# Kernel optimization log

Hardware: AMD Instinct MI355X
Metric: run time of the kernel (lower is better)

The kernel has to match this reference:

```python
import jax, jax.numpy as jnp
import numpy as np

B, L, E, H, V, NC = 64, 256, 300, 128, 50000, 2
NH1, F1 = 8, 8  # GAT layer 1: 8 heads x 8 features; layer 2: 1 head x 1 feature
LRELU = 0.2


def _lstm_dir(x, W, U, b):
    # x: [B, L, E]; W: [4H, E]; U: [4H, H]; b: [4H] (b_ih + b_hh fused)
    Bq, Hq = x.shape[0], U.shape[1]
    def step(carry, xt):
        h, c = carry
        g = xt @ W.T + h @ U.T + b
        i, f, gg, o = jnp.split(g, 4, axis=-1)  # PyTorch gate order i,f,g,o
        c = jax.nn.sigmoid(f) * c + jax.nn.sigmoid(i) * jnp.tanh(gg)
        h = jax.nn.sigmoid(o) * jnp.tanh(c)
        return (h, c), h
    h0 = jnp.zeros((Bq, Hq), x.dtype)
    _, hs = jax.lax.scan(step, (h0, h0), jnp.swapaxes(x, 0, 1))
    return jnp.swapaxes(hs, 0, 1)  # [B, L, H]


def bilstm(x, Wf, Uf, bf, Wb, Ub, bb):
    hf = _lstm_dir(x, Wf, Uf, bf)
    hb = _lstm_dir(x[:, ::-1], Wb, Ub, bb)[:, ::-1]
    return jnp.concatenate([hf, hb], axis=-1)  # [B, L, 2H]


def gat_layer(x, W, a_src, a_trg, bias, n_heads, f_out, concat, elu_act):
    # Dense equivalent of GAT IMP3 on a fully-connected graph (edge (s,t): src=s, trg=t).
    Bq, Lq, _ = x.shape
    proj = (x @ W.T).reshape(Bq, Lq, n_heads, f_out)        # [B,L,NH,F]
    s_src = jnp.einsum('blhf,hf->blh', proj, a_src)          # [B,L,NH]
    s_trg = jnp.einsum('blhf,hf->blh', proj, a_trg)
    sc = jax.nn.leaky_relu(s_src[:, :, None, :] + s_trg[:, None, :, :], LRELU)  # [B,S,T,NH]
    m = jnp.max(sc, axis=(1, 2, 3), keepdims=True)           # global max per graph (as in IMP3)
    e = jnp.exp(sc - m)
    A = e / (jnp.sum(e, axis=1, keepdims=True) + 1e-16)      # softmax over sources per target
    out = jnp.einsum('bsth,bshf->bthf', A, proj)             # scatter-aggregate to targets
    if concat:
        out = out.reshape(Bq, Lq, n_heads * f_out)
    else:
        out = out.mean(axis=2)
    out = out + bias
    if elu_act:
        out = jax.nn.elu(out)
    return out, A


def setup_inputs() -> dict:
    key = jax.random.key(0)
    ks = jax.random.split(key, 20)
    n = lambda k, shape, s=0.05: (jax.random.normal(k, shape, jnp.float32) * s)
    return {
        'input_ids': jax.random.randint(ks[0], (B, L), 0, V, jnp.int32),
        'attention_mask': jnp.ones((B, L), bool),
        'emb': n(ks[1], (V, E), 0.1),
        'Wih_f': n(ks[2], (4 * H, E)), 'Whh_f': n(ks[3], (4 * H, H)), 'b_f': jnp.zeros((4 * H,), jnp.float32),
        'Wih_b': n(ks[4], (4 * H, E)), 'Whh_b': n(ks[5], (4 * H, H)), 'b_b': jnp.zeros((4 * H,), jnp.float32),
        'g1_W': n(ks[6], (NH1 * F1, 2 * H)), 'g1_src': n(ks[7], (NH1, F1), 0.1), 'g1_trg': n(ks[8], (NH1, F1), 0.1), 'g1_b': jnp.zeros((NH1 * F1,), jnp.float32),
        'g2_W': n(ks[9], (1, NH1 * F1)), 'g2_src': n(ks[10], (1, 1), 0.1), 'g2_trg': n(ks[11], (1, 1), 0.1), 'g2_b': jnp.zeros((1,), jnp.float32),
        'ctx': n(ks[12], (L, 1), 0.1),
        'lin_W': n(ks[13], (B, 2 * H)), 'lin_b': jnp.zeros((B,), jnp.float32),
        'out_W': n(ks[14], (NC, B)), 'out_b': jnp.zeros((NC,), jnp.float32),
    }


def reference(input_ids, attention_mask, emb, Wih_f, Whh_f, b_f, Wih_b, Whh_b, b_b,
              g1_W, g1_src, g1_trg, g1_b, g2_W, g2_src, g2_trg, g2_b,
              ctx, lin_W, lin_b, out_W, out_b):
    x = emb[input_ids]                                   # [B,L,E] (dropout = eval no-op)
    h_seq = bilstm(x, Wih_f, Whh_f, b_f, Wih_b, Whh_b, b_b)  # [B,L,2H]
    h1, _ = gat_layer(h_seq, g1_W, g1_src, g1_trg, g1_b, NH1, F1, True, True)
    _, A2 = gat_layer(h1, g2_W, g2_src, g2_trg, g2_b, 1, 1, False, False)
    att2 = A2[..., 0]                                    # [B, src, trg] == att.view(-1, 2H) rows
    att = jnp.einsum('bst,t->bs', att2, ctx[:, 0])       # mm with context_vector
    att = jnp.where(attention_mask, att, -jnp.inf)
    att = jax.nn.softmax(att, axis=1)                    # [B,L]
    pooled = jnp.max(h_seq * att[..., None], axis=1)     # [B,2H]
    hcl = jax.nn.relu(pooled @ lin_W.T + lin_b)
    logits = hcl @ out_W.T + out_b                       # [B,NC]
    return (logits, att)
```

## Files before the change

### kernel.cpp

```cpp
#include <hip/hip_runtime.h>
#include <math.h>
#include <stdint.h>

#define Bq 64
#define Lq 256
#define Eq 300
#define Hq 128
#define MQ (Bq*Lq)

#define LRELU_S 0.2f

__device__ __forceinline__ float lrelu(float x) { return x > 0.f ? x : LRELU_S * x; }

typedef short short8 __attribute__((ext_vector_type(8)));
typedef float f32x4v __attribute__((ext_vector_type(4)));

__device__ __forceinline__ unsigned short f2bf(float x) {
  unsigned u = __float_as_uint(x);
  u += 0x7FFFu + ((u >> 16) & 1u);
  return (unsigned short)(u >> 16);
}
__device__ __forceinline__ float bf2f(unsigned short h) {
  return __uint_as_float(((unsigned)h) << 16);
}

#define BM 64
#define BN 64
#define BK 16

__global__ __launch_bounds__(256) void gemm_awt(
    const float* __restrict__ Asrc, const int* __restrict__ ids,
    const float* __restrict__ W, const float* __restrict__ bias,
    float* __restrict__ C, int M, int N, int K)
{
  __shared__ float As[BK][BM + 4];
  __shared__ float Bs[BK][BN + 4];
  int tid = threadIdx.x;
  int tx = tid & 15, ty = tid >> 4;
  int row0 = blockIdx.x * BM, col0 = blockIdx.y * BN;

  int lrow = tid >> 2;
  int lk   = (tid & 3) << 2;

  const float* Arow;
  {
    int r = row0 + lrow;
    int id = ids ? ids[r] : r;
    Arow = Asrc + (size_t)id * K;
  }
  const float* Wrow = W + (size_t)(col0 + lrow) * K;

  float acc[4][4] = {};

  for (int k0 = 0; k0 < K; k0 += BK) {
    int kk = k0 + lk;
    float4 av, bv;
    if (kk + 3 < K) {
      av = *(const float4*)(Arow + kk);
      bv = *(const float4*)(Wrow + kk);
    } else {
      float a0 = (kk + 0 < K) ? Arow[kk + 0] : 0.f;
      float a1 = (kk + 1 < K) ? Arow[kk + 1] : 0.f;
      float a2 = (kk + 2 < K) ? Arow[kk + 2] : 0.f;
      float a3 = (kk + 3 < K) ? Arow[kk + 3] : 0.f;
      av = make_float4(a0, a1, a2, a3);
      float b0 = (kk + 0 < K) ? Wrow[kk + 0] : 0.f;
      float b1 = (kk + 1 < K) ? Wrow[kk + 1] : 0.f;
      float b2 = (kk + 2 < K) ? Wrow[kk + 2] : 0.f;
      float b3 = (kk + 3 < K) ? Wrow[kk + 3] : 0.f;
      bv = make_float4(b0, b1, b2, b3);
    }
    As[lk + 0][lrow] = av.x; As[lk + 1][lrow] = av.y;
    As[lk + 2][lrow] = av.z; As[lk + 3][lrow] = av.w;
    Bs[lk + 0][lrow] = bv.x; Bs[lk + 1][lrow] = bv.y;
    Bs[lk + 2][lrow] = bv.z; Bs[lk + 3][lrow] = bv.w;
    __syncthreads();

    #pragma unroll
    for (int k = 0; k < BK; ++k) {
      float4 a4 = *(const float4*)&As[k][ty * 4];
      float4 b4 = *(const float4*)&Bs[k][tx * 4];
      float a[4] = {a4.x, a4.y, a4.z, a4.w};
      float bb[4] = {b4.x, b4.y, b4.z, b4.w};
      #pragma unroll
      for (int i = 0; i < 4; ++i)
        #pragma unroll
        for (int j = 0; j < 4; ++j)
          acc[i][j] += a[i] * bb[j];
    }
    __syncthreads();
  }

  #pragma unroll
  for (int i = 0; i < 4; ++i) {
    int r = row0 + ty * 4 + i;
    #pragma unroll
    for (int j = 0; j < 4; ++j) {
      int cidx = col0 + tx * 4 + j;
      float v = acc[i][j] + (bias ? bias[cidx] : 0.f);
      C[(size_t)r * N + cidx] = v;
    }
  }
}

__global__ __launch_bounds__(256) void gemm_gates_mfma(
    const float* __restrict__ emb, const int* __restrict__ ids,
    const float* __restrict__ Wf, const float* __restrict__ bf,
    const float* __restrict__ Wb, const float* __restrict__ bb_,
    float* __restrict__ C)
{
  __shared__ __align__(16) short Ah[128 * 32];
  __shared__ __align__(16) short Al[128 * 32];
  __shared__ __align__(16) short Bh[128 * 32];
  __shared__ __align__(16) short Bl[128 * 32];
  __shared__ int ids_s[128];

  int tid = threadIdx.x;
  int row0 = blockIdx.x * 128;
  int col0 = blockIdx.y * 128;
  const float* W    = (col0 < 512) ? Wf : Wb;
  const float* bias = (col0 < 512) ? bf : bb_;
  int wcol0 = col0 & 511;

  if (tid < 128) ids_s[tid] = ids[row0 + tid];
  __syncthreads();

  int l  = tid & 63, wv = tid >> 6;
  int wm = wv >> 1,  wn = wv & 1;
  int kq = l >> 4,   rl = l & 15;

  f32x4v acc[4][4] = {};

  for (int k0 = 0; k0 < 300; k0 += 32) {
    #pragma unroll
    for (int p = 0; p < 4; ++p) {
      int idx = p * 256 + tid;
      int row = idx >> 3, c4 = idx & 7;
      int gk = k0 + c4 * 4;
      float4 av = make_float4(0.f, 0.f, 0.f, 0.f);
      float4 bv = make_float4(0.f, 0.f, 0.f, 0.f);
      if (gk < 300) {
        av = *(const float4*)(emb + (size_t)ids_s[row] * 300 + gk);
        bv = *(const float4*)(W + (size_t)(wcol0 + row) * 300 + gk);
      }
      int chunk = (c4 >> 1) ^ ((row >> 2) & 3);
      int off = row * 32 + chunk * 8 + (c4 & 1) * 4;
      {
        unsigned short h0 = f2bf(av.x), h1 = f2bf(av.y), h2 = f2bf(av.z), h3 = f2bf(av.w);
        unsigned short l0 = f2bf(av.x - bf2f(h0)), l1 = f2bf(av.y - bf2f(h1));
        unsigned short l2 = f2bf(av.z - bf2f(h2)), l3 = f2bf(av.w - bf2f(h3));
        uint2 ph; ph.x = (unsigned)h0 | ((unsigned)h1 << 16); ph.y = (unsigned)h2 | ((unsigned)h3 << 16);
        uint2 pl; pl.x = (unsigned)l0 | ((unsigned)l1 << 16); pl.y = (unsigned)l2 | ((unsigned)l3 << 16);
        *(uint2*)&Ah[off] = ph;
        *(uint2*)&Al[off] = pl;
      }
      {
        unsigned short h0 = f2bf(bv.x), h1 = f2bf(bv.y), h2 = f2bf(bv.z), h3 = f2bf(bv.w);
        unsigned short l0 = f2bf(bv.x - bf2f(h0)), l1 = f2bf(bv.y - bf2f(h1));
        unsigned short l2 = f2bf(bv.z - bf2f(h2)), l3 = f2bf(bv.w - bf2f(h3));
        uint2 ph; ph.x = (unsigned)h0 | ((unsigned)h1 << 16); ph.y = (unsigned)h2 | ((unsigned)h3 << 16);
        uint2 pl; pl.x = (unsigned)l0 | ((unsigned)l1 << 16); pl.y = (unsigned)l2 | ((unsigned)l3 << 16);
        *(uint2*)&Bh[off] = ph;
        *(uint2*)&Bl[off] = pl;
      }
    }
    __syncthreads();

    short8 ah[4], al_[4], bh[4], bl[4];
    #pragma unroll
    for (int f = 0; f < 4; ++f) {
      int ar = wm * 64 + f * 16 + rl;
      int ac = kq ^ ((ar >> 2) & 3);
      ah[f]  = *(const short8*)&Ah[ar * 32 + ac * 8];
      al_[f] = *(const short8*)&Al[ar * 32 + ac * 8];
      int br = wn * 64 + f * 16 + rl;
      int bc = kq ^ ((br >> 2) & 3);
      bh[f]  = *(const short8*)&Bh[br * 32 + bc * 8];
      bl[f]  = *(const short8*)&Bl[br * 32 + bc * 8];
    }
    #pragma unroll
    for (int fm = 0; fm < 4; ++fm)
      #pragma unroll
      for (int fn = 0; fn < 4; ++fn) {
        acc[fm][fn] = __builtin_amdgcn_mfma_f32_16x16x32_bf16(ah[fm],  bh[fn], acc[fm][fn], 0, 0, 0);
        acc[fm][fn] = __builtin_amdgcn_mfma_f32_16x16x32_bf16(ah[fm],  bl[fn], acc[fm][fn], 0, 0, 0);
        acc[fm][fn] = __builtin_amdgcn_mfma_f32_16x16x32_bf16(al_[fm], bh[fn], acc[fm][fn], 0, 0, 0);
      }
    __syncthreads();
  }

  int fq = l >> 4;
  #pragma unroll
  for (int fm = 0; fm < 4; ++fm) {
    #pragma unroll
    for (int fn = 0; fn < 4; ++fn) {
      int gr = row0 + wm * 64 + fm * 16 + fq * 4;
      int lc = wn * 64 + fn * 16 + rl;
      float bsv = bias[wcol0 + lc];
      #pragma unroll
      for (int i = 0; i < 4; ++i)
        C[(size_t)(gr + i) * 1024 + col0 + lc] = acc[fm][fn][i] + bsv;
    }
  }
}

#define MVB(s0,s1,s2,s3, u0,u1,u2,u3, off) \
  "s_waitcnt lgkmcnt(5)\n" \
  "v_fmac_f32 v88, v" #s0 ", v" #u0 "\n" \
  "v_fmac_f32 v89, v" #s1 ", v" #u1 "\n" \
  "v_fmac_f32 v90, v" #s2 ", v" #u2 "\n" \
  "v_fmac_f32 v91, v" #s3 ", v" #u3 "\n" \
  "ds_read_b128 v[" #s0 ":" #s3 "], v81 offset:" #off "\n"

#define MVT(n, s0,s1,s2,s3, u0,u1,u2,u3) \
  "s_waitcnt lgkmcnt(" #n ")\n" \
  "v_fmac_f32 v88, v" #s0 ", v" #u0 "\n" \
  "v_fmac_f32 v89, v" #s1 ", v" #u1 "\n" \
  "v_fmac_f32 v90, v" #s2 ", v" #u2 "\n" \
  "v_fmac_f32 v91, v" #s3 ", v" #u3 "\n"

#define ULD(lo,hi,off) \
  "global_load_dwordx4 v[" #lo ":" #hi "], v80, %[ub] offset:" #off "\n"

__global__ __launch_bounds__(512, 1) void lstm_kernel(
    const float* __restrict__ ws_base,
    const float* __restrict__ Uf, const float* __restrict__ Ub,
    float* __restrict__ h_seq)
{
  __shared__ __align__(1024) float h_sh[2][Hq];
  int blk = blockIdx.x;
  int b = blk & 63;
  int dir = blk >> 6;
  int j = threadIdx.x;
  int lane = j & 63;
  int w = j >> 6;
  int gate = (lane >> 4) & 3;
  int hidx = (w << 4) | (lane & 15);
  int row = (gate << 7) | hidx;

  const float* U = dir ? Ub : Uf;
  int tt0 = dir ? (Lq - 1) : 0;

  unsigned uo  = (unsigned)row * (Hq * 4u);
  unsigned go0 = (1024u + (unsigned)(b * Lq + tt0) * 1024u
                  + (unsigned)dir * 512u + (unsigned)row) * 4u;
  unsigned ho0 = ((unsigned)(b * Lq + tt0) * 256u
                  + (unsigned)dir * (unsigned)Hq + (unsigned)hidx) * 4u;
  int gd = dir ? -4096 : 4096;
  int hd = dir ? -1024 : 1024;

  unsigned lds_base = (unsigned)(uintptr_t)&h_sh[0][0];
  unsigned ldsr0 = lds_base;
  unsigned ldsw0 = lds_base + 512u + (unsigned)hidx * 4u;

  bool isg = (gate == 2);
  float klog = isg ? -2.8853900817779268f : -1.4426950408889634f;
  float mc = isg ? 2.f : 1.f;
  float ac = isg ? -1.f : 0.f;
  int base4 = (lane & 15) * 4;
  int bp0 = base4, bp1 = base4 + 64, bp2 = base4 + 128, bp3 = base4 + 192;

  if (j < Hq) h_sh[0][j] = 0.f;
  __syncthreads();

  asm volatile(
    "v_mov_b32 v80, %[uo]\n"
    "v_mov_b32 v81, %[ldsr0]\n"
    "v_mov_b32 v82, %[ldsw0]\n"
    "v_mov_b32 v83, %[go0]\n"
    "v_mov_b32 v84, %[ho0]\n"
    "v_mov_b32 v87, 0\n"
    "s_mov_b32 s90, 0\n"
    ULD(128,131,0)   ULD(132,135,16)  ULD(136,139,32)  ULD(140,143,48)
    ULD(144,147,64)  ULD(148,151,80)  ULD(152,155,96)  ULD(156,159,112)
    ULD(160,163,128) ULD(164,167,144) ULD(168,171,160) ULD(172,175,176)
    ULD(176,179,192) ULD(180,183,208) ULD(184,187,224) ULD(188,191,240)
    ULD(192,195,256) ULD(196,199,272) ULD(200,203,288) ULD(204,207,304)
    ULD(208,211,320) ULD(212,215,336) ULD(216,219,352) ULD(220,223,368)
    ULD(224,227,384) ULD(228,231,400) ULD(232,235,416) ULD(236,239,432)
    ULD(240,243,448) ULD(244,247,464) ULD(248,251,480) ULD(252,255,496)
    "global_load_dword v85, v83, %[wsb]\n"
    "s_waitcnt vmcnt(0)\n"
    "Ltop_%=:\n"
    "v_add_u32 v83, %[gd], v83\n"
    "global_load_dword v86, v83, %[wsb]\n"
    "ds_read_b128 v[100:103], v81\n"
    "ds_read_b128 v[104:107], v81 offset:16\n"
    "ds_read_b128 v[108:111], v81 offset:32\n"
    "ds_read_b128 v[112:115], v81 offset:48\n"
    "ds_read_b128 v[116:119], v81 offset:64\n"
    "ds_read_b128 v[120:123], v81 offset:80\n"
    "v_mov_b32 v88, v85\n"
    "v_mov_b32 v89, 0\n"
    "v_mov_b32 v90, 0\n"
    "v_mov_b32 v91, 0\n"
    MVB(100,101,102,103, 128,129,130,131, 96)
    MVB(104,105,106,107, 132,133,134,135, 112)
    MVB(108,109,110,111, 136,137,138,139, 128)
    MVB(112,113,114,115, 140,141,142,143, 144)
    MVB(116,117,118,119, 144,145,146,147, 160)
    MVB(120,121,122,123, 148,149,150,151, 176)
    MVB(100,101,102,103, 152,153,154,155, 192)
    MVB(104,105,106,107, 156,157,158,159, 208)
    MVB(108,109,110,111, 160,161,162,163, 224)
    MVB(112,113,114,115, 164,165,166,167, 240)
    MVB(116,117,118,119, 168,169,170,171, 256)
    MVB(120,121,122,123, 172,173,174,175, 272)
    MVB(100,101,102,103, 176,177,178,179, 288)
    MVB(104,105,106,107, 180,181,182,183, 304)
    MVB(108,109,110,111, 184,185,186,187, 320)
    MVB(112,113,114,115, 188,189,190,191, 336)
    MVB(116,117,118,119, 192,193,194,195, 352)
    MVB(120,121,122,123, 196,197,198,199, 368)
    MVB(100,101,102,103, 200,201,202,203, 384)
    MVB(104,105,106,107, 204,205,206,207, 400)
    MVB(108,109,110,111, 208,209,210,211, 416)
    MVB(112,113,114,115, 212,213,214,215, 432)
    MVB(116,117,118,119, 216,217,218,219, 448)
    MVB(120,121,122,123, 220,221,222,223, 464)
    MVB(100,101,102,103, 224,225,226,227, 480)
    MVB(104,105,106,107, 228,229,230,231, 496)
    MVT(5, 108,109,110,111, 232,233,234,235)
    MVT(4, 112,113,114,115, 236,237,238,239)
    MVT(3, 116,117,118,119, 240,241,242,243)
    MVT(2, 120,121,122,123, 244,245,246,247)
    MVT(1, 100,101,102,103, 248,249,250,251)
    MVT(0, 104,105,106,107, 252,253,254,255)
    "v_add_f32 v88, v88, v90\n"
    "v_add_f32 v89, v89, v91\n"
    "v_add_f32 v88, v88, v89\n"
    "v_mul_f32 v92, %[klog], v88\n"
    "v_exp_f32 v93, v92\n"
    "s_nop 1\n"
    "v_add_f32 v94, 1.0, v93\n"
    "v_rcp_f32 v95, v94\n"
    "s_nop 1\n"
    "v_mul_f32 v96, v94, v95\n"
    "v_sub_f32 v96, 2.0, v96\n"
    "v_mul_f32 v95, v95, v96\n"
    "v_fma_f32 v97, v95, %[mc], %[ac]\n"
    "ds_bpermute_b32 v92, %[bp0], v97\n"
    "ds_bpermute_b32 v93, %[bp1], v97\n"
    "ds_bpermute_b32 v94, %[bp2], v97\n"
    "ds_bpermute_b32 v98, %[bp3], v97\n"
    "s_waitcnt lgkmcnt(0)\n"
    "v_mul_f32 v95, v92, v94\n"
    "v_fma_f32 v87, v93, v87, v95\n"
    "v_mul_f32 v92, 0xc038aa3b, v87\n"
    "v_exp_f32 v93, v92\n"
    "s_nop 1\n"
    "v_add_f32 v94, 1.0, v93\n"
    "v_rcp_f32 v95, v94\n"
    "s_nop 1\n"
    "v_mul_f32 v96, v94, v95\n"
    "v_sub_f32 v96, 2.0, v96\n"
    "v_mul_f32 v95, v95, v96\n"
    "v_fma_f32 v96, v95, 2.0, -1.0\n"
    "v_mul_f32 v96, v98, v96\n"
    "s_waitcnt vmcnt(0)\n"
    "v_mov_b32 v85, v86\n"
    "ds_write_b32 v82, v96\n"
    "global_store_dword v84, v96, %[hsb]\n"
    "v_add_u32 v84, %[hd], v84\n"
    "v_xor_b32 v81, 0x200, v81\n"
    "v_xor_b32 v82, 0x200, v82\n"
    "s_waitcnt lgkmcnt(0)\n"
    "s_barrier\n"
    "s_add_u32 s90, s90, 1\n"
    "s_cmp_lt_u32 s90, 256\n"
    "s_cbranch_scc1 Ltop_%=\n"
    "s_waitcnt vmcnt(0) lgkmcnt(0)\n"
    :
    : [wsb]"s"(ws_base), [hsb]"s"(h_seq), [ub]"s"(U),
      [gd]"s"(gd), [hd]"s"(hd),
      [uo]"v"(uo), [go0]"v"(go0), [ho0]"v"(ho0),
      [ldsr0]"v"(ldsr0), [ldsw0]"v"(ldsw0),
      [klog]"v"(klog), [mc]"v"(mc), [ac]"v"(ac),
      [bp0]"v"(bp0), [bp1]"v"(bp1), [bp2]"v"(bp2), [bp3]"v"(bp3)
    : "memory", "scc", "s90",
      "v80","v81","v82","v83","v84","v85","v86","v87","v88","v89",
      "v90","v91","v92","v93","v94","v95","v96","v97","v98",
      "v100","v101","v102","v103","v104","v105","v106","v107",
      "v108","v109","v110","v111","v112","v113","v114","v115",
      "v116","v117","v118","v119","v120","v121","v122","v123",
      "v128","v129","v130","v131","v132","v133","v134","v135",
      "v136","v137","v138","v139","v140","v141","v142","v143",
      "v144","v145","v146","v147","v148","v149","v150","v151",
      "v152","v153","v154","v155","v156","v157","v158","v159",
      "v160","v161","v162","v163","v164","v165","v166","v167",
      "v168","v169","v170","v171","v172","v173","v174","v175",
      "v176","v177","v178","v179","v180","v181","v182","v183",
      "v184","v185","v186","v187","v188","v189","v190","v191",
      "v192","v193","v194","v195","v196","v197","v198","v199",
      "v200","v201","v202","v203","v204","v205","v206","v207",
      "v208","v209","v210","v211","v212","v213","v214","v215",
      "v216","v217","v218","v219","v220","v221","v222","v223",
      "v224","v225","v226","v227","v228","v229","v230","v231",
      "v232","v233","v234","v235","v236","v237","v238","v239",
      "v240","v241","v242","v243","v244","v245","v246","v247",
      "v248","v249","v250","v251","v252","v253","v254","v255");
}
#undef MVB
#undef MVT
#undef ULD

__global__ void srctrg_kernel(const float* __restrict__ proj1,
                              const float* __restrict__ a_src,
                              const float* __restrict__ a_trg,
                              float* __restrict__ s_src, float* __restrict__ s_trg)
{
  int m = blockIdx.x * blockDim.x + threadIdx.x;
  if (m >= MQ) return;
  const float* p = proj1 + (size_t)m * 64;
  #pragma unroll
  for (int h = 0; h < 8; ++h) {
    float ss = 0.f, st = 0.f;
    #pragma unroll
    for (int f = 0; f < 8; ++f) {
      float v = p[h * 8 + f];
      ss += v * a_src[h * 8 + f];
      st += v * a_trg[h * 8 + f];
    }
    s_src[(size_t)m * 8 + h] = ss;
    s_trg[(size_t)m * 8 + h] = st;
  }
}

__global__ __launch_bounds__(256) void gat1max_kernel(
    const float* __restrict__ s_src, const float* __restrict__ s_trg,
    float* __restrict__ m1)
{
  int b = blockIdx.x;
  int tid = threadIdx.x;
  int h = tid >> 5, r = tid & 31;
  float ms = -3.4e38f, mt = -3.4e38f;
  for (int s = r; s < Lq; s += 32) {
    ms = fmaxf(ms, s_src[((size_t)b * Lq + s) * 8 + h]);
    mt = fmaxf(mt, s_trg[((size_t)b * Lq + s) * 8 + h]);
  }
  #pragma unroll
  for (int o = 16; o > 0; o >>= 1) {
    ms = fmaxf(ms, __shfl_xor(ms, o, 32));
    mt = fmaxf(mt, __shfl_xor(mt, o, 32));
  }
  __shared__ float hh[8];
  if (r == 0) hh[h] = ms + mt;
  __syncthreads();
  if (tid == 0) {
    float mm = -3.4e38f;
    #pragma unroll
    for (int k = 0; k < 8; ++k) mm = fmaxf(mm, hh[k]);
    m1[b] = lrelu(mm);
  }
}

__global__ __launch_bounds__(256) void gat1_agg_kernel(
    const float* __restrict__ s_src, const float* __restrict__ s_trg,
    const float* __restrict__ proj1, const float* __restrict__ m1,
    const float* __restrict__ g1_b, float* __restrict__ h1)
{
  int b = blockIdx.x >> 3;
  int h = blockIdx.x & 7;
  int t = threadIdx.x;
  __shared__ float src_s[Lq], trg_s[Lq];
  __shared__ float proj_s[Lq * 8];

  size_t base = (size_t)b * Lq;
  src_s[t] = s_src[(base + t) * 8 + h];
  trg_s[t] = s_trg[(base + t) * 8 + h];
  {
    const float4* pr = (const float4*)(proj1 + (base + t) * 64 + h * 8);
    float4* psh = (float4*)(proj_s + t * 8);
    psh[0] = pr[0];
    psh[1] = pr[1];
  }
  __syncthreads();

  float m = m1[b];
  float mytrg = trg_s[t];
  float den = 1e-16f;
  float acc[8] = {};
  for (int s = 0; s < Lq; ++s) {
    float w = __expf(lrelu(src_s[s] + mytrg) - m);
    den += w;
    const float* ps = proj_s + s * 8;
    #pragma unroll
    for (int f = 0; f < 8; ++f) acc[f] += w * ps[f];
  }
  float inv = 1.f / den;
  float* out = h1 + (base + t) * 64 + h * 8;
  #pragma unroll
  for (int f = 0; f < 8; ++f) {
    float v = acc[f] * inv + g1_b[h * 8 + f];
    out[f] = v > 0.f ? v : expm1f(v);
  }
}

__device__ __forceinline__ float block_max_256(float v, volatile float* red) {
  #pragma unroll
  for (int o = 32; o > 0; o >>= 1) v = fmaxf(v, __shfl_xor(v, o, 64));
  int tid = threadIdx.x;
  if ((tid & 63) == 0) red[tid >> 6] = v;
  __syncthreads();
  float r = fmaxf(fmaxf(red[0], red[1]), fmaxf(red[2], red[3]));
  __syncthreads();
  return r;
}
__device__ __forceinline__ float block_sum_256(float v, volatile float* red) {
  #pragma unroll
  for (int o = 32; o > 0; o >>= 1) v += __shfl_xor(v, o, 64);
  int tid = threadIdx.x;
  if ((tid & 63) == 0) red[tid >> 6] = v;
  __syncthreads();
  float r = red[0] + red[1] + red[2] + red[3];
  __syncthreads();
  return r;
}

__global__ __launch_bounds__(256) void gat2_att_pool_kernel(
    const float* __restrict__ h1, const float* __restrict__ g2_W,
    const float* __restrict__ g2_src, const float* __restrict__ g2_trg,
    const float* __restrict__ ctx, const float* __restrict__ h_seq,
    float* __restrict__ att_out, float* __restrict__ pooled)
{
  int b = blockIdx.x;
  int tid = threadIdx.x;
  __shared__ float w2[64];
  __shared__ float src2[Lq], trg2[Lq], dq[Lq], att_sh[Lq];
  __shared__ float red[4];

  if (tid < 64) w2[tid] = g2_W[tid];
  __syncthreads();

  const float* hr = h1 + ((size_t)b * Lq + tid) * 64;
  float p = 0.f;
  #pragma unroll
  for (int k = 0; k < 64; ++k) p += hr[k] * w2[k];
  float a_s = g2_src[0], a_t = g2_trg[0];
  src2[tid] = p * a_s;
  trg2[tid] = p * a_t;
  __syncthreads();

  float ms = block_max_256(src2[tid], red);
  float mt = block_max_256(trg2[tid], red);
  float m2 = lrelu(ms + mt);

  float mytrg = trg2[tid];
  float den = 1e-16f;
  for (int s = 0; s < Lq; ++s)
    den += __expf(lrelu(src2[s] + mytrg) - m2);
  dq[tid] = ctx[tid] / den;
  __syncthreads();

  float mysrc = src2[tid];
  float raw = 0.f;
  for (int t = 0; t < Lq; ++t)
    raw += dq[t] * __expf(lrelu(mysrc + trg2[t]) - m2);

  float mr = block_max_256(raw, red);
  float e = __expf(raw - mr);
  float ssum = block_sum_256(e, red);
  float att = e / ssum;
  att_out[(size_t)b * Lq + tid] = att;
  att_sh[tid] = att;
  __syncthreads();

  float pm = -3.4e38f;
  for (int l = 0; l < Lq; ++l)
    pm = fmaxf(pm, h_seq[((size_t)b * Lq + l) * 256 + tid] * att_sh[l]);
  pooled[(size_t)b * 256 + tid] = pm;
}

__global__ __launch_bounds__(256) void head_kernel(
    const float* __restrict__ pooled, const float* __restrict__ lin_W,
    const float* __restrict__ lin_b, const float* __restrict__ out_W,
    const float* __restrict__ out_b, float* __restrict__ logits)
{
  int i = blockIdx.x;
  int tid = threadIdx.x;
  int j = tid & 63, kq = tid >> 6;
  __shared__ float part[4][64];
  __shared__ float hcl[64];
  const float* pr = pooled + i * 256 + kq * 64;
  const float* wr = lin_W + j * 256 + kq * 64;
  float d = 0.f;
  #pragma unroll
  for (int k = 0; k < 64; ++k) d += pr[k] * wr[k];
  part[kq][j] = d;
  __syncthreads();
  if (tid < 64) {
    float v = part[0][j] + part[1][j] + part[2][j] + part[3][j] + lin_b[j];
    hcl[j] = fmaxf(v, 0.f);
  }
  __syncthreads();
  if (tid < 128) {
    int cc = tid >> 6, jj = tid & 63;
    float p = hcl[jj] * out_W[cc * 64 + jj];
    #pragma unroll
    for (int o = 32; o > 0; o >>= 1) p += __shfl_xor(p, o, 64);
    if (jj == 0) logits[i * 2 + cc] = p + out_b[cc];
  }
}

extern "C" void kernel_launch(void* const* d_in, const int* in_sizes, int n_in,
                              void* d_out, int out_size, void* d_ws, size_t ws_size,
                              hipStream_t stream)
{
  const int*   ids    = (const int*)  d_in[0];
  const float* emb    = (const float*)d_in[2];
  const float* Wih_f  = (const float*)d_in[3];
  const float* Whh_f  = (const float*)d_in[4];
  const float* b_f    = (const float*)d_in[5];
  const float* Wih_b  = (const float*)d_in[6];
  const float* Whh_b  = (const float*)d_in[7];
  const float* b_b    = (const float*)d_in[8];
  const float* g1_W   = (const float*)d_in[9];
  const float* g1_src = (const float*)d_in[10];
  const float* g1_trg = (const float*)d_in[11];
  const float* g1_b   = (const float*)d_in[12];
  const float* g2_W   = (const float*)d_in[13];
  const float* g2_src = (const float*)d_in[14];
  const float* g2_trg = (const float*)d_in[15];
  const float* ctx    = (const float*)d_in[17];
  const float* lin_W  = (const float*)d_in[18];
  const float* lin_b  = (const float*)d_in[19];
  const float* out_W  = (const float*)d_in[20];
  const float* out_b  = (const float*)d_in[21];

  float* out_f   = (float*)d_out;
  float* logits  = out_f;
  float* att_out = out_f + 128;

  float* ws = (float*)d_ws;
  const size_t M = MQ;
  float* ws_base = ws;
  ws += 1024;
  float* gates   = ws; ws += M * 1024;
  float* h_seq   = ws; ws += M * 256;
  float* proj1   = ws; ws += M * 64;
  float* s_src   = ws; ws += M * 8;
  float* s_trg   = ws; ws += M * 8;
  float* h1      = ws; ws += M * 64;
  float* m1      = ws; ws += 64;
  float* pooled  = ws; ws += 64 * 256;

  dim3 thr(256);

  gemm_gates_mfma<<<dim3(MQ / 128, 1024 / 128), thr, 0, stream>>>(emb, ids, Wih_f, b_f, Wih_b, b_b, gates);

  lstm_kernel<<<128, 512, 0, stream>>>(ws_base, Whh_f, Whh_b, h_seq);

  gemm_awt<<<dim3(MQ / BM, 1), thr, 0, stream>>>(h_seq, nullptr, g1_W, nullptr, proj1, MQ, 64, 256);
  srctrg_kernel<<<MQ / 256, thr, 0, stream>>>(proj1, g1_src, g1_trg, s_src, s_trg);
  gat1max_kernel<<<Bq, thr, 0, stream>>>(s_src, s_trg, m1);
  gat1_agg_kernel<<<Bq * 8, thr, 0, stream>>>(s_src, s_trg, proj1, m1, g1_b, h1);

  gat2_att_pool_kernel<<<Bq, thr, 0, stream>>>(h1, g2_W, g2_src, g2_trg, ctx, h_seq, att_out, pooled);

  head_kernel<<<64, thr, 0, stream>>>(pooled, lin_W, lin_b, out_W, out_b, logits);
}
```

Baseline: 363.4 us.

## Broadcast LSTM hidden state via scalar loads from global instead of LDS

The recurrent LSTM loop no longer keeps the hidden state in LDS; each step reads the previous h vector from the h_seq output in global memory with s_load_dwordx16 into SGPRs after invalidating the scalar cache, and uses SGPR operands in the FMAs. This removes the LDS write/read and the ds_read waits from the serial critical path, and a tiny kernel zeroes a 128-float region used as the initial h. The trade-off is that each step now depends on a global store becoming visible and on a scalar-cache refill, and it relies on store/barrier ordering across waves being enough for the scalar loads to see fresh data.

```diff
diff --git a/kernel.cpp b/kernel.cpp
--- a/kernel.cpp
+++ b/kernel.cpp
@@ -23,6 +23,8 @@
 __device__ __forceinline__ float bf2f(unsigned short h) {
   return __uint_as_float(((unsigned)h) << 16);
 }
+
+__global__ void zero128(float* __restrict__ p) { p[threadIdx.x] = 0.f; }
 
 #define BM 64
 #define BN 64
@@ -204,30 +206,152 @@
   }
 }
 
-#define MVB(s0,s1,s2,s3, u0,u1,u2,u3, off) \
-  "s_waitcnt lgkmcnt(5)\n" \
-  "v_fmac_f32 v88, v" #s0 ", v" #u0 "\n" \
-  "v_fmac_f32 v89, v" #s1 ", v" #u1 "\n" \
-  "v_fmac_f32 v90, v" #s2 ", v" #u2 "\n" \
-  "v_fmac_f32 v91, v" #s3 ", v" #u3 "\n" \
-  "ds_read_b128 v[" #s0 ":" #s3 "], v81 offset:" #off "\n"
-
-#define MVT(n, s0,s1,s2,s3, u0,u1,u2,u3) \
-  "s_waitcnt lgkmcnt(" #n ")\n" \
-  "v_fmac_f32 v88, v" #s0 ", v" #u0 "\n" \
-  "v_fmac_f32 v89, v" #s1 ", v" #u1 "\n" \
-  "v_fmac_f32 v90, v" #s2 ", v" #u2 "\n" \
-  "v_fmac_f32 v91, v" #s3 ", v" #u3 "\n"
+#define FMQ(s0,u0,s1,u1,s2,u2,s3,u3) \
+  "v_fmac_f32 v88, s" #s0 ", v" #u0 "\n" \
+  "v_fmac_f32 v89, s" #s1 ", v" #u1 "\n" \
+  "v_fmac_f32 v90, s" #s2 ", v" #u2 "\n" \
+  "v_fmac_f32 v91, s" #s3 ", v" #u3 "\n"
 
 #define ULD(lo,hi,off) \
   "global_load_dwordx4 v[" #lo ":" #hi "], v80, %[ub] offset:" #off "\n"
+
+#define LSTM_ASM(GDS, HDS, HDHIS) \
+  asm volatile( \
+    "v_mov_b32 v80, %[uo]\n" \
+    "v_mov_b32 v83, %[go0]\n" \
+    "v_mov_b32 v84, %[ho0]\n" \
+    "v_mov_b32 v87, 0\n" \
+    "s_mov_b32 s88, 0\n" \
+    "s_mov_b64 s[90:91], %[hz]\n" \
+    ULD(128,131,0)   ULD(132,135,16)  ULD(136,139,32)  ULD(140,143,48) \
+    ULD(144,147,64)  ULD(148,151,80)  ULD(152,155,96)  ULD(156,159,112) \
+    ULD(160,163,128) ULD(164,167,144) ULD(168,171,160) ULD(172,175,176) \
+    ULD(176,179,192) ULD(180,183,208) ULD(184,187,224) ULD(188,191,240) \
+    ULD(192,195,256) ULD(196,199,272) ULD(200,203,288) ULD(204,207,304) \
+    ULD(208,211,320) ULD(212,215,336) ULD(216,219,352) ULD(220,223,368) \
+    ULD(224,227,384) ULD(228,231,400) ULD(232,235,416) ULD(236,239,432) \
+    ULD(240,243,448) ULD(244,247,464) ULD(248,251,480) ULD(252,255,496) \
+    "global_load_dword v85, v83, %[wsb]\n" \
+    "s_waitcnt vmcnt(0)\n" \
+    "Ltop_%=:\n" \
+    "v_add_u32 v83, " GDS ", v83\n" \
+    "global_load_dword v86, v83, %[wsb]\n" \
+    "s_dcache_inv\n" \
+    "s_load_dwordx16 s[0:15],  s[90:91], 0x0\n" \
+    "s_load_dwordx16 s[16:31], s[90:91], 0x40\n" \
+    "s_load_dwordx16 s[32:47], s[90:91], 0x80\n" \
+    "s_load_dwordx16 s[48:63], s[90:91], 0xC0\n" \
+    "v_mov_b32 v88, v85\n" \
+    "v_mov_b32 v89, 0\n" \
+    "v_mov_b32 v90, 0\n" \
+    "v_mov_b32 v91, 0\n" \
+    "s_waitcnt lgkmcnt(0)\n" \
+    FMQ(0,128, 1,129, 2,130, 3,131)   FMQ(4,132, 5,133, 6,134, 7,135) \
+    FMQ(8,136, 9,137, 10,138, 11,139) FMQ(12,140, 13,141, 14,142, 15,143) \
+    FMQ(16,144, 17,145, 18,146, 19,147) FMQ(20,148, 21,149, 22,150, 23,151) \
+    FMQ(24,152, 25,153, 26,154, 27,155) FMQ(28,156, 29,157, 30,158, 31,159) \
+    FMQ(32,160, 33,161, 34,162, 35,163) FMQ(36,164, 37,165, 38,166, 39,167) \
+    FMQ(40,168, 41,169, 42,170, 43,171) FMQ(44,172, 45,173, 46,174, 47,175) \
+    FMQ(48,176, 49,177, 50,178, 51,179) FMQ(52,180, 53,181, 54,182, 55,183) \
+    FMQ(56,184, 57,185, 58,186, 59,187) FMQ(60,188, 61,189, 62,190, 63,191) \
+    "s_load_dwordx16 s[0:15],  s[90:91], 0x100\n" \
+    "s_load_dwordx16 s[16:31], s[90:91], 0x140\n" \
+    "s_load_dwordx16 s[32:47], s[90:91], 0x180\n" \
+    "s_load_dwordx16 s[48:63], s[90:91], 0x1C0\n" \
+    "s_waitcnt lgkmcnt(0)\n" \
+    FMQ(0,192, 1,193, 2,194, 3,195)   FMQ(4,196, 5,197, 6,198, 7,199) \
+    FMQ(8,200, 9,201, 10,202, 11,203) FMQ(12,204, 13,205, 14,206, 15,207) \
+    FMQ(16,208, 17,209, 18,210, 19,211) FMQ(20,212, 21,213, 22,214, 23,215) \
+    FMQ(24,216, 25,217, 26,218, 27,219) FMQ(28,220, 29,221, 30,222, 31,223) \
+    FMQ(32,224, 33,225, 34,226, 35,227) FMQ(36,228, 37,229, 38,230, 39,231) \
+    FMQ(40,232, 41,233, 42,234, 43,235) FMQ(44,236, 45,237, 46,238, 47,239) \
+    FMQ(48,240, 49,241, 50,242, 51,243) FMQ(52,244, 53,245, 54,246, 55,247) \
+    FMQ(56,248, 57,249, 58,250, 59,251) FMQ(60,252, 61,253, 62,254, 63,255) \
+    "v_add_f32 v88, v88, v90\n" \
+    "v_add_f32 v89, v89, v91\n" \
+    "v_add_f32 v88, v88, v89\n" \
+    "v_mul_f32 v92, %[klog], v88\n" \
+    "v_exp_f32 v93, v92\n" \
+    "s_nop 1\n" \
+    "v_add_f32 v94, 1.0, v93\n" \
+    "v_rcp_f32 v95, v94\n" \
+    "s_nop 1\n" \
+    "v_mul_f32 v96, v94, v95\n" \
+    "v_sub_f32 v96, 2.0, v96\n" \
+    "v_mul_f32 v95, v95, v96\n" \
+    "v_fma_f32 v97, v95, %[mc], %[ac]\n" \
+    "ds_bpermute_b32 v92, %[bp0], v97\n" \
+    "ds_bpermute_b32 v93, %[bp1], v97\n" \
+    "ds_bpermute_b32 v94, %[bp2], v97\n" \
+    "ds_bpermute_b32 v98, %[bp3], v97\n" \
+    "s_waitcnt lgkmcnt(0)\n" \
+    "v_mul_f32 v95, v92, v94\n" \
+    "v_fma_f32 v87, v93, v87, v95\n" \
+    "v_mul_f32 v92, 0xc038aa3b, v87\n" \
+    "v_exp_f32 v93, v92\n" \
+    "s_nop 1\n" \
+    "v_add_f32 v94, 1.0, v93\n" \
+    "v_rcp_f32 v95, v94\n" \
+    "s_nop 1\n" \
+    "v_mul_f32 v96, v94, v95\n" \
+    "v_sub_f32 v96, 2.0, v96\n" \
+    "v_mul_f32 v95, v95, v96\n" \
+    "v_fma_f32 v96, v95, 2.0, -1.0\n" \
+    "v_mul_f32 v96, v98, v96\n" \
+    "s_waitcnt vmcnt(0)\n" \
+    "v_mov_b32 v85, v86\n" \
+    "global_store_dword v84, v96, %[hsb]\n" \
+    "v_add_u32 v84, " HDS ", v84\n" \
+    "s_waitcnt vmcnt(0)\n" \
+    "s_barrier\n" \
+    "s_add_u32 s90, s90, " HDS "\n" \
+    "s_addc_u32 s91, s91, " HDHIS "\n" \
+    "s_cmp_eq_u32 s88, 0\n" \
+    "s_cselect_b64 s[90:91], %[hr0], s[90:91]\n" \
+    "s_add_u32 s88, s88, 1\n" \
+    "s_cmp_lt_u32 s88, 256\n" \
+    "s_cbranch_scc1 Ltop_%=\n" \
+    "s_waitcnt vmcnt(0) lgkmcnt(0)\n" \
+    : \
+    : [wsb]"s"(ws_base), [hsb]"s"(h_seq), [ub]"s"(U), \
+      [hz]"s"(hz), [hr0]"s"(hr0), \
+      [uo]"v"(uo), [go0]"v"(go0), [ho0]"v"(ho0), \
+      [klog]"v"(klog), [mc]"v"(mc), [ac]"v"(ac), \
+      [bp0]"v"(bp0), [bp1]"v"(bp1), [bp2]"v"(bp2), [bp3]"v"(bp3) \
+    : "memory", "scc", \
+      "s0","s1","s2","s3","s4","s5","s6","s7", \
+      "s8","s9","s10","s11","s12","s13","s14","s15", \
+      "s16","s17","s18","s19","s20","s21","s22","s23", \
+      "s24","s25","s26","s27","s28","s29","s30","s31", \
+      "s32","s33","s34","s35","s36","s37","s38","s39", \
+      "s40","s41","s42","s43","s44","s45","s46","s47", \
+      "s48","s49","s50","s51","s52","s53","s54","s55", \
+      "s56","s57","s58","s59","s60","s61","s62","s63", \
+      "s88","s90","s91", \
+      "v80","v83","v84","v85","v86","v87","v88","v89", \
+      "v90","v91","v92","v93","v94","v95","v96","v97","v98", \
+      "v128","v129","v130","v131","v132","v133","v134","v135", \
+      "v136","v137","v138","v139","v140","v141","v142","v143", \
+      "v144","v145","v146","v147","v148","v149","v150","v151", \
+      "v152","v153","v154","v155","v156","v157","v158","v159", \
+      "v160","v161","v162","v163","v164","v165","v166","v167", \
+      "v168","v169","v170","v171","v172","v173","v174","v175", \
+      "v176","v177","v178","v179","v180","v181","v182","v183", \
+      "v184","v185","v186","v187","v188","v189","v190","v191", \
+      "v192","v193","v194","v195","v196","v197","v198","v199", \
+      "v200","v201","v202","v203","v204","v205","v206","v207", \
+      "v208","v209","v210","v211","v212","v213","v214","v215", \
+      "v216","v217","v218","v219","v220","v221","v222","v223", \
+      "v224","v225","v226","v227","v228","v229","v230","v231", \
+      "v232","v233","v234","v235","v236","v237","v238","v239", \
+      "v240","v241","v242","v243","v244","v245","v246","v247", \
+      "v248","v249","v250","v251","v252","v253","v254","v255")
 
 __global__ __launch_bounds__(512, 1) void lstm_kernel(
     const float* __restrict__ ws_base,
     const float* __restrict__ Uf, const float* __restrict__ Ub,
     float* __restrict__ h_seq)
 {
-  __shared__ __align__(1024) float h_sh[2][Hq];
   int blk = blockIdx.x;
   int b = blk & 63;
   int dir = blk >> 6;
@@ -246,12 +370,10 @@
                   + (unsigned)dir * 512u + (unsigned)row) * 4u;
   unsigned ho0 = ((unsigned)(b * Lq + tt0) * 256u
                   + (unsigned)dir * (unsigned)Hq + (unsigned)hidx) * 4u;
-  int gd = dir ? -4096 : 4096;
-  int hd = dir ? -1024 : 1024;
-
-  unsigned lds_base = (unsigned)(uintptr_t)&h_sh[0][0];
-  unsigned ldsr0 = lds_base;
-  unsigned ldsw0 = lds_base + 512u + (unsigned)hidx * 4u;
+
+  unsigned long long hz  = (unsigned long long)(uintptr_t)ws_base;
+  unsigned long long hr0 = (unsigned long long)(uintptr_t)h_seq
+      + (((unsigned long long)(b * Lq + tt0) * 256ull + (unsigned long long)dir * Hq) * 4ull);
 
   bool isg = (gate == 2);
   float klog = isg ? -2.8853900817779268f : -1.4426950408889634f;
@@ -260,149 +382,15 @@
   int base4 = (lane & 15) * 4;
   int bp0 = base4, bp1 = base4 + 64, bp2 = base4 + 128, bp3 = base4 + 192;
 
-  if (j < Hq) h_sh[0][j] = 0.f;
-  __syncthreads();
-
-  asm volatile(
-    "v_mov_b32 v80, %[uo]\n"
-    "v_mov_b32 v81, %[ldsr0]\n"
-    "v_mov_b32 v82, %[ldsw0]\n"
-    "v_mov_b32 v83, %[go0]\n"
-    "v_mov_b32 v84, %[ho0]\n"
-    "v_mov_b32 v87, 0\n"
-    "s_mov_b32 s90, 0\n"
-    ULD(128,131,0)   ULD(132,135,16)  ULD(136,139,32)  ULD(140,143,48)
-    ULD(144,147,64)  ULD(148,151,80)  ULD(152,155,96)  ULD(156,159,112)
-    ULD(160,163,128) ULD(164,167,144) ULD(168,171,160) ULD(172,175,176)
-    ULD(176,179,192) ULD(180,183,208) ULD(184,187,224) ULD(188,191,240)
-    ULD(192,195,256) ULD(196,199,272) ULD(200,203,288) ULD(204,207,304)
-    ULD(208,211,320) ULD(212,215,336) ULD(216,219,352) ULD(220,223,368)
-    ULD(224,227,384) ULD(228,231,400) ULD(232,235,416) ULD(236,239,432)
-    ULD(240,243,448) ULD(244,247,464) ULD(248,251,480) ULD(252,255,496)
-    "global_load_dword v85, v83, %[wsb]\n"
-    "s_waitcnt vmcnt(0)\n"
-    "Ltop_%=:\n"
-    "v_add_u32 v83, %[gd], v83\n"
-    "global_load_dword v86, v83, %[wsb]\n"
-    "ds_read_b128 v[100:103], v81\n"
-    "ds_read_b128 v[104:107], v81 offset:16\n"
-    "ds_read_b128 v[108:111], v81 offset:32\n"
-    "ds_read_b128 v[112:115], v81 offset:48\n"
-    "ds_read_b128 v[116:119], v81 offset:64\n"
-    "ds_read_b128 v[120:123], v81 offset:80\n"
-    "v_mov_b32 v88, v85\n"
-    "v_mov_b32 v89, 0\n"
-    "v_mov_b32 v90, 0\n"
-    "v_mov_b32 v91, 0\n"
-    MVB(100,101,102,103, 128,129,130,131, 96)
-    MVB(104,105,106,107, 132,133,134,135, 112)
-    MVB(108,109,110,111, 136,137,138,139, 128)
-    MVB(112,113,114,115, 140,141,142,143, 144)
-    MVB(116,117,118,119, 144,145,146,147, 160)
-    MVB(120,121,122,123, 148,149,150,151, 176)
-    MVB(100,101,102,103, 152,153,154,155, 192)
-    MVB(104,105,106,107, 156,157,158,159, 208)
-    MVB(108,109,110,111, 160,161,162,163, 224)
-    MVB(112,113,114,115, 164,165,166,167, 240)
-    MVB(116,117,118,119, 168,169,170,171, 256)
-    MVB(120,121,122,123, 172,173,174,175, 272)
-    MVB(100,101,102,103, 176,177,178,179, 288)
-    MVB(104,105,106,107, 180,181,182,183, 304)
-    MVB(108,109,110,111, 184,185,186,187, 320)
-    MVB(112,113,114,115, 188,189,190,191, 336)
-    MVB(116,117,118,119, 192,193,194,195, 352)
-    MVB(120,121,122,123, 196,197,198,199, 368)
-    MVB(100,101,102,103, 200,201,202,203, 384)
-    MVB(104,105,106,107, 204,205,206,207, 400)
-    MVB(108,109,110,111, 208,209,210,211, 416)
-    MVB(112,113,114,115, 212,213,214,215, 432)
-    MVB(116,117,118,119, 216,217,218,219, 448)
-    MVB(120,121,122,123, 220,221,222,223, 464)
-    MVB(100,101,102,103, 224,225,226,227, 480)
-    MVB(104,105,106,107, 228,229,230,231, 496)
-    MVT(5, 108,109,110,111, 232,233,234,235)
-    MVT(4, 112,113,114,115, 236,237,238,239)
-    MVT(3, 116,117,118,119, 240,241,242,243)
-    MVT(2, 120,121,122,123, 244,245,246,247)
-    MVT(1, 100,101,102,103, 248,249,250,251)
-    MVT(0, 104,105,106,107, 252,253,254,255)
-    "v_add_f32 v88, v88, v90\n"
-    "v_add_f32 v89, v89, v91\n"
-    "v_add_f32 v88, v88, v89\n"
-    "v_mul_f32 v92, %[klog], v88\n"
-    "v_exp_f32 v93, v92\n"
-    "s_nop 1\n"
-    "v_add_f32 v94, 1.0, v93\n"
-    "v_rcp_f32 v95, v94\n"
-    "s_nop 1\n"
-    "v_mul_f32 v96, v94, v95\n"
-    "v_sub_f32 v96, 2.0, v96\n"
-    "v_mul_f32 v95, v95, v96\n"
-    "v_fma_f32 v97, v95, %[mc], %[ac]\n"
-    "ds_bpermute_b32 v92, %[bp0], v97\n"
-    "ds_bpermute_b32 v93, %[bp1], v97\n"
-    "ds_bpermute_b32 v94, %[bp2], v97\n"
-    "ds_bpermute_b32 v98, %[bp3], v97\n"
-    "s_waitcnt lgkmcnt(0)\n"
-    "v_mul_f32 v95, v92, v94\n"
-    "v_fma_f32 v87, v93, v87, v95\n"
-    "v_mul_f32 v92, 0xc038aa3b, v87\n"
-    "v_exp_f32 v93, v92\n"
-    "s_nop 1\n"
-    "v_add_f32 v94, 1.0, v93\n"
-    "v_rcp_f32 v95, v94\n"
-    "s_nop 1\n"
-    "v_mul_f32 v96, v94, v95\n"
-    "v_sub_f32 v96, 2.0, v96\n"
-    "v_mul_f32 v95, v95, v96\n"
-    "v_fma_f32 v96, v95, 2.0, -1.0\n"
-    "v_mul_f32 v96, v98, v96\n"
-    "s_waitcnt vmcnt(0)\n"
-    "v_mov_b32 v85, v86\n"
-    "ds_write_b32 v82, v96\n"
-    "global_store_dword v84, v96, %[hsb]\n"
-    "v_add_u32 v84, %[hd], v84\n"
-    "v_xor_b32 v81, 0x200, v81\n"
-    "v_xor_b32 v82, 0x200, v82\n"
-    "s_waitcnt lgkmcnt(0)\n"
-    "s_barrier\n"
-    "s_add_u32 s90, s90, 1\n"
-    "s_cmp_lt_u32 s90, 256\n"
-    "s_cbranch_scc1 Ltop_%=\n"
-    "s_waitcnt vmcnt(0) lgkmcnt(0)\n"
-    :
-    : [wsb]"s"(ws_base), [hsb]"s"(h_seq), [ub]"s"(U),
-      [gd]"s"(gd), [hd]"s"(hd),
-      [uo]"v"(uo), [go0]"v"(go0), [ho0]"v"(ho0),
-      [ldsr0]"v"(ldsr0), [ldsw0]"v"(ldsw0),
-      [klog]"v"(klog), [mc]"v"(mc), [ac]"v"(ac),
-      [bp0]"v"(bp0), [bp1]"v"(bp1), [bp2]"v"(bp2), [bp3]"v"(bp3)
-    : "memory", "scc", "s90",
-      "v80","v81","v82","v83","v84","v85","v86","v87","v88","v89",
-      "v90","v91","v92","v93","v94","v95","v96","v97","v98",
-      "v100","v101","v102","v103","v104","v105","v106","v107",
-      "v108","v109","v110","v111","v112","v113","v114","v115",
-      "v116","v117","v118","v119","v120","v121","v122","v123",
-      "v128","v129","v130","v131","v132","v133","v134","v135",
-      "v136","v137","v138","v139","v140","v141","v142","v143",
-      "v144","v145","v146","v147","v148","v149","v150","v151",
-      "v152","v153","v154","v155","v156","v157","v158","v159",
-      "v160","v161","v162","v163","v164","v165","v166","v167",
-      "v168","v169","v170","v171","v172","v173","v174","v175",
-      "v176","v177","v178","v179","v180","v181","v182","v183",
-      "v184","v185","v186","v187","v188","v189","v190","v191",
-      "v192","v193","v194","v195","v196","v197","v198","v199",
-      "v200","v201","v202","v203","v204","v205","v206","v207",
-      "v208","v209","v210","v211","v212","v213","v214","v215",
-      "v216","v217","v218","v219","v220","v221","v222","v223",
-      "v224","v225","v226","v227","v228","v229","v230","v231",
-      "v232","v233","v234","v235","v236","v237","v238","v239",
-      "v240","v241","v242","v243","v244","v245","v246","v247",
-      "v248","v249","v250","v251","v252","v253","v254","v255");
-}
-#undef MVB
-#undef MVT
+  if (dir == 0) {
+    LSTM_ASM("4096", "1024", "0");
+  } else {
+    LSTM_ASM("0xfffff000", "0xfffffc00", "-1");
+  }
+}
+#undef FMQ
 #undef ULD
+#undef LSTM_ASM
 
 __global__ void srctrg_kernel(const float* __restrict__ proj1,
                               const float* __restrict__ a_src,
@@ -646,6 +634,8 @@
 
   dim3 thr(256);
 
+  zero128<<<1, 128, 0, stream>>>(ws_base);
+
   gemm_gates_mfma<<<dim3(MQ / 128, 1024 / 128), thr, 0, stream>>>(emb, ids, Wih_f, b_f, Wih_b, b_b, gates);
 
   lstm_kernel<<<128, 512, 0, stream>>>(ws_base, Whh_f, Whh_b, h_seq);
```

Result: slower. 563.1 us (+54.9%).

## Fuse GAT1 score, max and aggregate kernels; fold head into GAT2 pooling

Applied to the files above, without the earlier changes.

The separate source/target score kernel, the per-graph max kernel and the GAT1 aggregation kernel become one kernel. Each block now computes its head's scores from proj1 and takes a block-level max. The MLP head is folded into the GAT2 attention/pooling kernel, and the inner exp/max loops are unrolled four-way with split accumulators for more instruction-level parallelism. This removes three launches and the s_src/s_trg/m1/pooled round-trips through global memory. The stabilizing max is now per head rather than global across heads, which cancels mathematically in the softmax but slightly changes numerical behaviour.

```diff
diff --git a/kernel.cpp b/kernel.cpp
--- a/kernel.cpp
+++ b/kernel.cpp
@@ -404,88 +404,72 @@
 #undef MVT
 #undef ULD
 
-__global__ void srctrg_kernel(const float* __restrict__ proj1,
-                              const float* __restrict__ a_src,
-                              const float* __restrict__ a_trg,
-                              float* __restrict__ s_src, float* __restrict__ s_trg)
-{
-  int m = blockIdx.x * blockDim.x + threadIdx.x;
-  if (m >= MQ) return;
-  const float* p = proj1 + (size_t)m * 64;
+__device__ __forceinline__ float block_max_256(float v, volatile float* red) {
   #pragma unroll
-  for (int h = 0; h < 8; ++h) {
-    float ss = 0.f, st = 0.f;
-    #pragma unroll
-    for (int f = 0; f < 8; ++f) {
-      float v = p[h * 8 + f];
-      ss += v * a_src[h * 8 + f];
-      st += v * a_trg[h * 8 + f];
-    }
-    s_src[(size_t)m * 8 + h] = ss;
-    s_trg[(size_t)m * 8 + h] = st;
-  }
-}
-
-__global__ __launch_bounds__(256) void gat1max_kernel(
-    const float* __restrict__ s_src, const float* __restrict__ s_trg,
-    float* __restrict__ m1)
-{
-  int b = blockIdx.x;
+  for (int o = 32; o > 0; o >>= 1) v = fmaxf(v, __shfl_xor(v, o, 64));
   int tid = threadIdx.x;
-  int h = tid >> 5, r = tid & 31;
-  float ms = -3.4e38f, mt = -3.4e38f;
-  for (int s = r; s < Lq; s += 32) {
-    ms = fmaxf(ms, s_src[((size_t)b * Lq + s) * 8 + h]);
-    mt = fmaxf(mt, s_trg[((size_t)b * Lq + s) * 8 + h]);
-  }
+  if ((tid & 63) == 0) red[tid >> 6] = v;
+  __syncthreads();
+  float r = fmaxf(fmaxf(red[0], red[1]), fmaxf(red[2], red[3]));
+  __syncthreads();
+  return r;
+}
+__device__ __forceinline__ float block_sum_256(float v, volatile float* red) {
   #pragma unroll
-  for (int o = 16; o > 0; o >>= 1) {
-    ms = fmaxf(ms, __shfl_xor(ms, o, 32));
-    mt = fmaxf(mt, __shfl_xor(mt, o, 32));
-  }
-  __shared__ float hh[8];
-  if (r == 0) hh[h] = ms + mt;
-  __syncthreads();
-  if (tid == 0) {
-    float mm = -3.4e38f;
-    #pragma unroll
-    for (int k = 0; k < 8; ++k) mm = fmaxf(mm, hh[k]);
-    m1[b] = lrelu(mm);
-  }
-}
-
-__global__ __launch_bounds__(256) void gat1_agg_kernel(
-    const float* __restrict__ s_src, const float* __restrict__ s_trg,
-    const float* __restrict__ proj1, const float* __restrict__ m1,
-    const float* __restrict__ g1_b, float* __restrict__ h1)
+  for (int o = 32; o > 0; o >>= 1) v += __shfl_xor(v, o, 64);
+  int tid = threadIdx.x;
+  if ((tid & 63) == 0) red[tid >> 6] = v;
+  __syncthreads();
+  float r = red[0] + red[1] + red[2] + red[3];
+  __syncthreads();
+  return r;
+}
+
+__global__ __launch_bounds__(256) void gat1_fused_kernel(
+    const float* __restrict__ proj1, const float* __restrict__ g1_src,
+    const float* __restrict__ g1_trg, const float* __restrict__ g1_b,
+    float* __restrict__ h1)
 {
   int b = blockIdx.x >> 3;
   int h = blockIdx.x & 7;
   int t = threadIdx.x;
   __shared__ float src_s[Lq], trg_s[Lq];
   __shared__ float proj_s[Lq * 8];
+  __shared__ float red[4];
 
   size_t base = (size_t)b * Lq;
-  src_s[t] = s_src[(base + t) * 8 + h];
-  trg_s[t] = s_trg[(base + t) * 8 + h];
+  float pv[8];
   {
     const float4* pr = (const float4*)(proj1 + (base + t) * 64 + h * 8);
+    float4 p0 = pr[0], p1 = pr[1];
+    pv[0]=p0.x; pv[1]=p0.y; pv[2]=p0.z; pv[3]=p0.w;
+    pv[4]=p1.x; pv[5]=p1.y; pv[6]=p1.z; pv[7]=p1.w;
     float4* psh = (float4*)(proj_s + t * 8);
-    psh[0] = pr[0];
-    psh[1] = pr[1];
-  }
-  __syncthreads();
-
-  float m = m1[b];
+    psh[0] = p0; psh[1] = p1;
+  }
+  float ss = 0.f, st = 0.f;
+  #pragma unroll
+  for (int f = 0; f < 8; ++f) {
+    ss += pv[f] * g1_src[h * 8 + f];
+    st += pv[f] * g1_trg[h * 8 + f];
+  }
+  src_s[t] = ss;
+  trg_s[t] = st;
+  __syncthreads();
+
+  float ms = block_max_256(ss, red);
+  float mt = block_max_256(st, red);
+  float m = lrelu(ms + mt);
+
   float mytrg = trg_s[t];
   float den = 1e-16f;
   float acc[8] = {};
   for (int s = 0; s < Lq; ++s) {
-    float w = __expf(lrelu(src_s[s] + mytrg) - m);
-    den += w;
+    float wgt = __expf(lrelu(src_s[s] + mytrg) - m);
+    den += wgt;
     const float* ps = proj_s + s * 8;
     #pragma unroll
-    for (int f = 0; f < 8; ++f) acc[f] += w * ps[f];
+    for (int f = 0; f < 8; ++f) acc[f] += wgt * ps[f];
   }
   float inv = 1.f / den;
   float* out = h1 + (base + t) * 64 + h * 8;
@@ -496,38 +480,21 @@
   }
 }
 
-__device__ __forceinline__ float block_max_256(float v, volatile float* red) {
-  #pragma unroll
-  for (int o = 32; o > 0; o >>= 1) v = fmaxf(v, __shfl_xor(v, o, 64));
-  int tid = threadIdx.x;
-  if ((tid & 63) == 0) red[tid >> 6] = v;
-  __syncthreads();
-  float r = fmaxf(fmaxf(red[0], red[1]), fmaxf(red[2], red[3]));
-  __syncthreads();
-  return r;
-}
-__device__ __forceinline__ float block_sum_256(float v, volatile float* red) {
-  #pragma unroll
-  for (int o = 32; o > 0; o >>= 1) v += __shfl_xor(v, o, 64);
-  int tid = threadIdx.x;
-  if ((tid & 63) == 0) red[tid >> 6] = v;
-  __syncthreads();
-  float r = red[0] + red[1] + red[2] + red[3];
-  __syncthreads();
-  return r;
-}
-
-__global__ __launch_bounds__(256) void gat2_att_pool_kernel(
+__global__ __launch_bounds__(256) void gat2_pool_head_kernel(
     const float* __restrict__ h1, const float* __restrict__ g2_W,
     const float* __restrict__ g2_src, const float* __restrict__ g2_trg,
     const float* __restrict__ ctx, const float* __restrict__ h_seq,
-    float* __restrict__ att_out, float* __restrict__ pooled)
+    const float* __restrict__ lin_W, const float* __restrict__ lin_b,
+    const float* __restrict__ out_W, const float* __restrict__ out_b,
+    float* __restrict__ att_out, float* __restrict__ logits)
 {
   int b = blockIdx.x;
   int tid = threadIdx.x;
   __shared__ float w2[64];
-  __shared__ float src2[Lq], trg2[Lq], dq[Lq], att_sh[Lq];
+  __shared__ float src2[Lq], trg2[Lq], dq[Lq], att_sh[Lq], pool_sh[256];
   __shared__ float red[4];
+  __shared__ float part[4][64];
+  __shared__ float hcl[64];
 
   if (tid < 64) w2[tid] = g2_W[tid];
   __syncthreads();
@@ -546,16 +513,25 @@
   float m2 = lrelu(ms + mt);
 
   float mytrg = trg2[tid];
-  float den = 1e-16f;
-  for (int s = 0; s < Lq; ++s)
-    den += __expf(lrelu(src2[s] + mytrg) - m2);
-  dq[tid] = ctx[tid] / den;
+  float d0 = 1e-16f, d1 = 0.f, d2 = 0.f, d3 = 0.f;
+  for (int s = 0; s < Lq; s += 4) {
+    d0 += __expf(lrelu(src2[s + 0] + mytrg) - m2);
+    d1 += __expf(lrelu(src2[s + 1] + mytrg) - m2);
+    d2 += __expf(lrelu(src2[s + 2] + mytrg) - m2);
+    d3 += __expf(lrelu(src2[s + 3] + mytrg) - m2);
+  }
+  dq[tid] = ctx[tid] / ((d0 + d1) + (d2 + d3));
   __syncthreads();
 
   float mysrc = src2[tid];
-  float raw = 0.f;
-  for (int t = 0; t < Lq; ++t)
-    raw += dq[t] * __expf(lrelu(mysrc + trg2[t]) - m2);
+  float r0 = 0.f, r1 = 0.f, r2 = 0.f, r3 = 0.f;
+  for (int t = 0; t < Lq; t += 4) {
+    r0 += dq[t + 0] * __expf(lrelu(mysrc + trg2[t + 0]) - m2);
+    r1 += dq[t + 1] * __expf(lrelu(mysrc + trg2[t + 1]) - m2);
+    r2 += dq[t + 2] * __expf(lrelu(mysrc + trg2[t + 2]) - m2);
+    r3 += dq[t + 3] * __expf(lrelu(mysrc + trg2[t + 3]) - m2);
+  }
+  float raw = (r0 + r1) + (r2 + r3);
 
   float mr = block_max_256(raw, red);
   float e = __expf(raw - mr);
@@ -566,39 +542,38 @@
   __syncthreads();
 
   float pm = -3.4e38f;
-  for (int l = 0; l < Lq; ++l)
-    pm = fmaxf(pm, h_seq[((size_t)b * Lq + l) * 256 + tid] * att_sh[l]);
-  pooled[(size_t)b * 256 + tid] = pm;
-}
-
-__global__ __launch_bounds__(256) void head_kernel(
-    const float* __restrict__ pooled, const float* __restrict__ lin_W,
-    const float* __restrict__ lin_b, const float* __restrict__ out_W,
-    const float* __restrict__ out_b, float* __restrict__ logits)
-{
-  int i = blockIdx.x;
-  int tid = threadIdx.x;
-  int j = tid & 63, kq = tid >> 6;
-  __shared__ float part[4][64];
-  __shared__ float hcl[64];
-  const float* pr = pooled + i * 256 + kq * 64;
-  const float* wr = lin_W + j * 256 + kq * 64;
-  float d = 0.f;
-  #pragma unroll
-  for (int k = 0; k < 64; ++k) d += pr[k] * wr[k];
-  part[kq][j] = d;
+  const float* hb = h_seq + (size_t)b * Lq * 256 + tid;
+  for (int l = 0; l < Lq; l += 4) {
+    float v0 = hb[(size_t)(l + 0) * 256] * att_sh[l + 0];
+    float v1 = hb[(size_t)(l + 1) * 256] * att_sh[l + 1];
+    float v2 = hb[(size_t)(l + 2) * 256] * att_sh[l + 2];
+    float v3 = hb[(size_t)(l + 3) * 256] * att_sh[l + 3];
+    pm = fmaxf(pm, fmaxf(fmaxf(v0, v1), fmaxf(v2, v3)));
+  }
+  pool_sh[tid] = pm;
+  __syncthreads();
+
+  {
+    int jj = tid & 63, kq = tid >> 6;
+    const float* pr = pool_sh + kq * 64;
+    const float* wr = lin_W + jj * 256 + kq * 64;
+    float d = 0.f;
+    #pragma unroll
+    for (int k = 0; k < 64; ++k) d += pr[k] * wr[k];
+    part[kq][jj] = d;
+  }
   __syncthreads();
   if (tid < 64) {
-    float v = part[0][j] + part[1][j] + part[2][j] + part[3][j] + lin_b[j];
-    hcl[j] = fmaxf(v, 0.f);
+    float v = part[0][tid] + part[1][tid] + part[2][tid] + part[3][tid] + lin_b[tid];
+    hcl[tid] = fmaxf(v, 0.f);
   }
   __syncthreads();
   if (tid < 128) {
     int cc = tid >> 6, jj = tid & 63;
-    float p = hcl[jj] * out_W[cc * 64 + jj];
-    #pragma unroll
-    for (int o = 32; o > 0; o >>= 1) p += __shfl_xor(p, o, 64);
-    if (jj == 0) logits[i * 2 + cc] = p + out_b[cc];
+    float pp = hcl[jj] * out_W[cc * 64 + jj];
+    #pragma unroll
+    for (int o = 32; o > 0; o >>= 1) pp += __shfl_xor(pp, o, 64);
+    if (jj == 0) logits[b * 2 + cc] = pp + out_b[cc];
   }
 }
 
@@ -638,11 +613,7 @@
   float* gates   = ws; ws += M * 1024;
   float* h_seq   = ws; ws += M * 256;
   float* proj1   = ws; ws += M * 64;
-  float* s_src   = ws; ws += M * 8;
-  float* s_trg   = ws; ws += M * 8;
   float* h1      = ws; ws += M * 64;
-  float* m1      = ws; ws += 64;
-  float* pooled  = ws; ws += 64 * 256;
 
   dim3 thr(256);
 
@@ -651,11 +622,9 @@
   lstm_kernel<<<128, 512, 0, stream>>>(ws_base, Whh_f, Whh_b, h_seq);
 
   gemm_awt<<<dim3(MQ / BM, 1), thr, 0, stream>>>(h_seq, nullptr, g1_W, nullptr, proj1, MQ, 64, 256);
-  srctrg_kernel<<<MQ / 256, thr, 0, stream>>>(proj1, g1_src, g1_trg, s_src, s_trg);
-  gat1max_kernel<<<Bq, thr, 0, stream>>>(s_src, s_trg, m1);
-  gat1_agg_kernel<<<Bq * 8, thr, 0, stream>>>(s_src, s_trg, proj1, m1, g1_b, h1);
-
-  gat2_att_pool_kernel<<<Bq, thr, 0, stream>>>(h1, g2_W, g2_src, g2_trg, ctx, h_seq, att_out, pooled);
-
-  head_kernel<<<64, thr, 0, stream>>>(pooled, lin_W, lin_b, out_W, out_b, logits);
-}
+  gat1_fused_kernel<<<Bq * 8, thr, 0, stream>>>(proj1, g1_src, g1_trg, g1_b, h1);
+
+  gat2_pool_head_kernel<<<Bq, thr, 0, stream>>>(h1, g2_W, g2_src, g2_trg, ctx, h_seq,
+                                                lin_W, lin_b, out_W, out_b,
+                                                att_out, logits);
+}
```

Result: faster. 326.1 us (-10.3%).
